# Kernel tuning notes

Measured on AMD Instinct MI355X. Metric: run time of the kernel, lower is better.

The kernel has to match this reference:

```python
import jax, jax.numpy as jnp
import numpy as np

N, NJ, K, F = 30000, 12, 32, 128


def _resmlp(x, wr, br, w1, b1):
    # Residual: x + Linear(SiLU(x)); then ResMLP head: Linear(SiLU(.))
    h = x + jax.nn.silu(x) @ wr.T + br
    return jax.nn.silu(h) @ w1.T + b1


def setup_inputs() -> dict:
    key = jax.random.key(0)
    ks = jax.random.split(key, 40)
    d = {}
    d["atom_fea"] = jax.random.normal(ks[0], (N, F), jnp.float32)
    d["nbr_fea_idx"] = jax.random.randint(ks[1], (N, NJ), 0, N)
    d["gs"] = jax.random.normal(ks[2], (N, NJ, K), jnp.float32)
    d["gp"] = jax.random.normal(ks[3], (N, NJ, K, 3), jnp.float32)
    d["gd"] = jax.random.normal(ks[4], (N, NJ, K, 5), jnp.float32)
    # parameters (nn.init.uniform_ default is U[0,1); scaled down for stability)
    d["Gs"] = jax.random.uniform(ks[5], (F, K), jnp.float32) * 0.1
    d["Gp"] = jax.random.uniform(ks[6], (F, K), jnp.float32) * 0.1
    d["Gd"] = jax.random.uniform(ks[7], (F, K), jnp.float32) * 0.1
    d["P1"] = jax.random.uniform(ks[8], (F, F), jnp.float32) * 0.02
    d["P2"] = jax.random.uniform(ks[9], (F, F), jnp.float32) * 0.02
    d["D1"] = jax.random.uniform(ks[10], (F, F), jnp.float32) * 0.02
    d["D2"] = jax.random.uniform(ks[11], (F, F), jnp.float32) * 0.02
    i = 12
    for name in ("c", "s", "p", "d"):
        d[name + "_wr"] = jax.random.normal(ks[i], (F, F), jnp.float32) * 0.05; i += 1
        d[name + "_br"] = jnp.zeros((F,), jnp.float32)
        d[name + "_w1"] = jax.random.normal(ks[i], (F, F), jnp.float32) * 0.05; i += 1
        d[name + "_b1"] = jnp.zeros((F,), jnp.float32)
    return d


def reference(atom_fea, nbr_fea_idx, gs, gp, gd,
              Gs, Gp, Gd, P1, P2, D1, D2,
              c_wr, c_br, c_w1, c_b1,
              s_wr, s_br, s_w1, s_b1,
              p_wr, p_br, p_w1, p_b1,
              d_wr, d_br, d_w1, d_b1):
    s_fea = _resmlp(atom_fea, s_wr, s_br, s_w1, s_b1)  # (N,F)
    p_fea = _resmlp(atom_fea, p_wr, p_br, p_w1, p_b1)
    d_fea = _resmlp(atom_fea, d_wr, d_br, d_w1, d_b1)

    # s channel: env_j = Gs @ gs_j, si = sum_j s_fea[nbr_j] * env_j
    env_s = jnp.einsum('fk,njk->njf', Gs, gs)                 # (N,NJ,F)
    final_s = jnp.sum(s_fea[nbr_fea_idx] * env_s, axis=1)     # (N,F)

    # p channel: (N,F,3) per-atom, then trace((P2^T p^T)(p P1)) = sum(pP1 * pP2)
    env_p = jnp.einsum('fk,njka->njfa', Gp, gp)               # (N,NJ,F,3)
    all_p = jnp.sum(p_fea[nbr_fea_idx][..., None] * env_p, axis=1)  # (N,F,3)
    all_p = jnp.swapaxes(all_p, 1, 2)                          # (N,3,F)
    p1 = jnp.einsum('naf,fg->nag', all_p, P1)
    p2 = jnp.einsum('naf,fg->nag', all_p, P2)
    final_p = jnp.sum(p1 * p2, axis=(1, 2))[:, None]           # (N,1) -> bcast (N,F)

    # d channel: same with 5 components
    env_d = jnp.einsum('fk,njka->njfa', Gd, gd)               # (N,NJ,F,5)
    all_d = jnp.sum(d_fea[nbr_fea_idx][..., None] * env_d, axis=1)  # (N,F,5)
    all_d = jnp.swapaxes(all_d, 1, 2)                          # (N,5,F)
    d1 = jnp.einsum('naf,fg->nag', all_d, D1)
    d2 = jnp.einsum('naf,fg->nag', all_d, D2)
    final_d = jnp.sum(d1 * d2, axis=(1, 2))[:, None]

    final_c = _resmlp(atom_fea, c_wr, c_br, c_w1, c_b1)        # (N,F)
    return final_c + final_s + final_p + final_d
```

## Files before the change

### kernel.cpp

```cpp
#include <hip/hip_runtime.h>

#define N_ATOMS 30000
#define NJ 12
#define FDIM 128

typedef __attribute__((ext_vector_type(8))) short short8;
typedef __attribute__((ext_vector_type(4))) float f32x4;

#define WFRAG_OFF 0
#define GFRAG_OFF 262144
#define MFRAG_OFF 286720
#define FEA_OFF   483328
#define FEA_ELEMS 3840000
#define ALLP_OFF  23523328
#define ALLD_OFF  46563328
#define QP_OFF    84963328
#define QD_OFF    85323328

__device__ __forceinline__ unsigned pack_bf2(float a, float b){
  unsigned r;
  asm("v_cvt_pk_bf16_f32 %0, %1, %2" : "=v"(r) : "v"(a), "v"(b));
  return r;
}
__device__ __forceinline__ unsigned short f2b(float f){
  return (unsigned short)pack_bf2(f, 0.f);
}
__device__ __forceinline__ float b2f(unsigned short s){
  unsigned u = ((unsigned)s) << 16;
  return __builtin_bit_cast(float, u);
}
__device__ __forceinline__ float silu_f(float x){ return x / (1.0f + __expf(-x)); }
__device__ __forceinline__ void lds_fence(){
  __builtin_amdgcn_sched_barrier(0);
  asm volatile("s_waitcnt lgkmcnt(0)" ::: "memory");
  __builtin_amdgcn_sched_barrier(0);
}
__device__ __forceinline__ short8 frag4(unsigned d0, unsigned d1, unsigned d2, unsigned d3, bool valid){
  if (!valid){ d0 = 0u; d1 = 0u; d2 = 0u; d3 = 0u; }
  uint4 u; u.x = d0; u.y = d1; u.z = d2; u.w = d3;
  return __builtin_bit_cast(short8, u);
}

struct Ptr8 { const float* p[8]; };
struct Ptr3 { const float* p[3]; };
struct Bias { const float* br[4]; const float* b1[4]; };

__global__ __launch_bounds__(256) void k_prep(
    const float* __restrict__ P1, const float* __restrict__ P2,
    const float* __restrict__ D1, const float* __restrict__ D2,
    Ptr8 w8, Ptr3 g3, char* __restrict__ ws)
{
  int b = blockIdx.x, t = threadIdx.x;
  if (b < 16){
    int mat = b >> 3, rb = b & 7;
    const float* A = mat ? D1 : P1;
    const float* B = mat ? D2 : P2;
    unsigned short* dst = (unsigned short*)(ws + MFRAG_OFF) + (size_t)mat*16384;
    for (int it = 0; it < 8; ++it){
      int o = it*256 + t;
      int row = rb*16 + (o >> 7), col = o & 127;
      const float4* ar = (const float4*)(A + (size_t)row*128);
      const float4* br = (const float4*)(B + (size_t)col*128);
      float s = 0.f;
      #pragma unroll 8
      for (int q = 0; q < 32; ++q){
        float4 a = ar[q], c = br[q];
        s += a.x*c.x + a.y*c.y + a.z*c.z + a.w*c.w;
      }
      int ks = row >> 5, ft = col >> 4;
      int ln = (col & 15) | (((row >> 3) & 3) << 4);
      dst[(size_t)(((ks*8 + ft)*64 + ln)*8 + (row & 7))] = f2b(s);
    }
  } else if (b < 24){
    int mat = b - 16;
    const float* W = w8.p[mat];
    unsigned short* dst = (unsigned short*)(ws + WFRAG_OFF) + (size_t)mat*16384;
    for (int it = 0; it < 64; ++it){
      int idx = it*256 + t;
      int i = idx & 7, ln = (idx >> 3) & 63, ft = (idx >> 9) & 7, ks = idx >> 12;
      int f = ft*16 + (ln & 15);
      int k = ks*32 + ((ln >> 4) & 3)*8 + i;
      dst[idx] = f2b(W[(size_t)f*128 + k]);
    }
  } else {
    int mat = b - 24;
    const float* G = g3.p[mat];
    unsigned short* dst = (unsigned short*)(ws + GFRAG_OFF) + (size_t)mat*4096;
    for (int it = 0; it < 16; ++it){
      int idx = it*256 + t;
      int i = idx & 7, ln = (idx >> 3) & 63, ft = idx >> 9;
      int f = ft*16 + (ln & 15);
      int k = ((ln >> 4) & 3)*8 + i;
      dst[idx] = f2b(G[(size_t)f*32 + k]);
    }
  }
}

__global__ __launch_bounds__(256) void k_resmlp(
    const float* __restrict__ x, char* __restrict__ ws, Bias bs,
    float* __restrict__ out)
{
  __shared__ alignas(16) char sm[32768];
  const int tid = threadIdx.x, lane = tid & 63;
  const int wid = __builtin_amdgcn_readfirstlane(tid >> 6);
  const int lo = lane & 15, hi = lane >> 4;
  const int ch = blockIdx.y;
  const int rowbase = (int)blockIdx.x*64 + wid*16;
  char* xL = sm + wid*8192;
  char* hL = xL + 4096;

  #pragma unroll
  for (int it = 0; it < 8; ++it){
    int e4 = it*64 + lane;
    int row = e4 >> 5, k0 = (e4 & 31)*4;
    int grow = rowbase + row; if (grow >= N_ATOMS) grow = N_ATOMS-1;
    float4 v = *(const float4*)(x + (size_t)grow*FDIM + k0);
    uint2 u;
    u.x = pack_bf2(silu_f(v.x), silu_f(v.y));
    u.y = pack_bf2(silu_f(v.z), silu_f(v.w));
    int ks = k0 >> 5, h2 = (k0 >> 3) & 3, i0 = k0 & 7, lanep = row | (h2 << 4);
    *(uint2*)(xL + ks*1024 + lanep*16 + i0*2) = u;
  }
  lds_fence();
  short8 A[4];
  #pragma unroll
  for (int ks = 0; ks < 4; ++ks) A[ks] = *(const short8*)(xL + ks*1024 + lane*16);

  const char* wrp = ws + (size_t)(ch*2)*32768;
  const char* w1p = ws + (size_t)(ch*2 + 1)*32768;
  const float* brp = bs.br[ch];
  const float* b1p = bs.b1[ch];

  f32x4 acc[8];
  #pragma unroll
  for (int ft = 0; ft < 8; ++ft) acc[ft] = (f32x4){0.f,0.f,0.f,0.f};
  #pragma unroll
  for (int ks = 0; ks < 4; ++ks){
    #pragma unroll
    for (int ft = 0; ft < 8; ++ft){
      short8 B = *(const short8*)(wrp + (size_t)(((ks*8 + ft)*64 + lane)*16));
      acc[ft] = __builtin_amdgcn_mfma_f32_16x16x32_bf16(A[ks], B, acc[ft], 0, 0, 0);
    }
  }
  #pragma unroll
  for (int ft = 0; ft < 8; ++ft){
    int f = ft*16 + lo;
    float bias = brp[f];
    #pragma unroll
    for (int r = 0; r < 4; ++r){
      int grow = rowbase + hi*4 + r; if (grow >= N_ATOMS) grow = N_ATOMS-1;
      float h = acc[ft][r] + x[(size_t)grow*FDIM + f] + bias;
      float sh = silu_f(h);
      int ks2 = f >> 5, h2 = (f >> 3) & 3, i2 = f & 7, lanep = (hi*4 + r) | (h2 << 4);
      *(unsigned short*)(hL + ks2*1024 + lanep*16 + i2*2) = f2b(sh);
    }
  }
  lds_fence();
  short8 A2[4];
  #pragma unroll
  for (int ks = 0; ks < 4; ++ks) A2[ks] = *(const short8*)(hL + ks*1024 + lane*16);

  f32x4 acc2[8];
  #pragma unroll
  for (int ft = 0; ft < 8; ++ft) acc2[ft] = (f32x4){0.f,0.f,0.f,0.f};
  #pragma unroll
  for (int ks = 0; ks < 4; ++ks){
    #pragma unroll
    for (int ft = 0; ft < 8; ++ft){
      short8 B = *(const short8*)(w1p + (size_t)(((ks*8 + ft)*64 + lane)*16));
      acc2[ft] = __builtin_amdgcn_mfma_f32_16x16x32_bf16(A2[ks], B, acc2[ft], 0, 0, 0);
    }
  }
  if (ch == 0){
    #pragma unroll
    for (int ft = 0; ft < 8; ++ft){
      int f = ft*16 + lo;
      float bb = b1p[f];
      #pragma unroll
      for (int r = 0; r < 4; ++r){
        int grow = rowbase + hi*4 + r; if (grow >= N_ATOMS) grow = N_ATOMS-1;
        out[(size_t)grow*FDIM + f] = acc2[ft][r] + bb;
      }
    }
  } else {
    unsigned short* fea = (unsigned short*)(ws + FEA_OFF) + (size_t)(ch-1)*FEA_ELEMS;
    #pragma unroll
    for (int ft = 0; ft < 8; ++ft){
      int f = ft*16 + lo;
      float bb = b1p[f];
      #pragma unroll
      for (int r = 0; r < 4; ++r){
        int grow = rowbase + hi*4 + r; if (grow >= N_ATOMS) grow = N_ATOMS-1;
        fea[(size_t)grow*FDIM + f] = f2b(acc2[ft][r] + bb);
      }
    }
  }
}

#define FPAD 264
#define SLABROWS 40
#define SLAB (SLABROWS*FPAD)

__device__ __forceinline__ void stage_fea(char* buf, const unsigned short* fea,
                                          int nb, int lane)
{
  #pragma unroll
  for (int j = 0; j < NJ; ++j){
    int nj = __builtin_amdgcn_readlane(nb, j);
    const unsigned* rp = (const unsigned*)(fea + (size_t)nj*FDIM);
    unsigned v = rp[lane];
    *(unsigned*)(buf + j*FPAD + lane*4) = v;
  }
}

__global__ __launch_bounds__(256, 4) void k_chan(
    const float* __restrict__ gs, const float* __restrict__ gp,
    const float* __restrict__ gd, const int* __restrict__ nbr,
    char* __restrict__ ws, float* __restrict__ out)
{
  __shared__ alignas(16) char sm[4*SLAB];
  const int tid = threadIdx.x, lane = tid & 63;
  const int wid = __builtin_amdgcn_readfirstlane(tid >> 6);
  const int lo = lane & 15, hi = lane >> 4;
  const bool jvalid = lo < NJ;
  const int jc = jvalid ? lo : NJ-1;
  char* slab = sm + wid*SLAB;
  const int atom = (int)blockIdx.x*4 + wid;
  const f32x4 z4 = {0.f,0.f,0.f,0.f};
  const unsigned short* feaS = (const unsigned short*)(ws + FEA_OFF);
  const char* gfrag = ws + GFRAG_OFF;

  int nb = 0;
  if (lane < NJ) nb = nbr[(size_t)atom*NJ + lane];

  #pragma unroll
  for (int t = 0; t < 4; ++t)
    *(float*)(slab + 36*FPAD + (t*64 + lane)*4) = 0.f;
  if (lane < 8) *(float*)(slab + 36*FPAD + 1024 + lane*4) = 0.f;

  stage_fea(slab,            feaS,               nb, lane);
  stage_fea(slab + 12*FPAD,  feaS + FEA_ELEMS,   nb, lane);
  stage_fea(slab + 24*FPAD,  feaS + 2*FEA_ELEMS, nb, lane);

  const float* gsp = gs + (size_t)atom*384 + (jc*32 + hi*8);
  f32x4 sv0 = *(const f32x4*)(gsp);
  f32x4 sv1 = *(const f32x4*)(gsp + 4);
  const float* gpp = gp + (size_t)atom*1152 + (jc*96 + hi*24);
  float pr[24];
  #pragma unroll
  for (int q = 0; q < 6; ++q){
    f32x4 v = *(const f32x4*)(gpp + q*4);
    #pragma unroll
    for (int c2 = 0; c2 < 4; ++c2) pr[q*4+c2] = v[c2];
  }

  const char* a0s = slab + hi*(4*FPAD) + lo*2;

  lds_fence();

  {
    short8 AfS = frag4(pack_bf2(sv0[0],sv0[1]), pack_bf2(sv0[2],sv0[3]),
                       pack_bf2(sv1[0],sv1[1]), pack_bf2(sv1[2],sv1[3]), jvalid);
    short8 Bg[8];
    #pragma unroll
    for (int ft = 0; ft < 8; ++ft)
      Bg[ft] = *(const short8*)(gfrag + (size_t)((ft*64 + lane)*16));
    float outv0 = 0.f, outv1 = 0.f;
    #pragma unroll
    for (int ft = 0; ft < 8; ++ft){
      float w0 = b2f(*(const unsigned short*)(a0s + 0*FPAD + ft*32));
      float w1 = b2f(*(const unsigned short*)(a0s + 1*FPAD + ft*32));
      float w2 = b2f(*(const unsigned short*)(a0s + 2*FPAD + ft*32));
      float w3 = b2f(*(const unsigned short*)(a0s + 3*FPAD + ft*32));
      f32x4 c = __builtin_amdgcn_mfma_f32_16x16x32_bf16(AfS, Bg[ft], z4, 0, 0, 0);
      float p = c[0]*w0 + c[1]*w1 + c[2]*w2 + c[3]*w3;
      p += __shfl_xor(p, 16);
      p += __shfl_xor(p, 32);
      if (ft == hi)     outv0 += p;
      if (ft == hi + 4) outv1 += p;
    }
    size_t ob = (size_t)atom*FDIM;
    out[ob + lane]      += outv0;
    out[ob + 64 + lane] += outv1;
  }

  const float* gdp = gd + (size_t)atom*1920 + (jc*160 + hi*40);
  float dr[40];
  #pragma unroll
  for (int q = 0; q < 10; ++q){
    f32x4 v = *(const f32x4*)(gdp + q*4);
    #pragma unroll
    for (int c2 = 0; c2 < 4; ++c2) dr[q*4+c2] = v[c2];
  }

  {
    unsigned short* allp = (unsigned short*)(ws + ALLP_OFF);
    short8 AfP[3];
    #pragma unroll
    for (int a = 0; a < 3; ++a)
      AfP[a] = frag4(pack_bf2(pr[0+a],pr[3+a]),   pack_bf2(pr[6+a],pr[9+a]),
                     pack_bf2(pr[12+a],pr[15+a]), pack_bf2(pr[18+a],pr[21+a]), jvalid);
    short8 Bg[8];
    #pragma unroll
    for (int ft = 0; ft < 8; ++ft)
      Bg[ft] = *(const short8*)(gfrag + 8192 + (size_t)((ft*64 + lane)*16));
    const char* a0 = a0s + 12*FPAD;
    #pragma unroll
    for (int ft = 0; ft < 8; ++ft){
      float w0 = b2f(*(const unsigned short*)(a0 + 0*FPAD + ft*32));
      float w1 = b2f(*(const unsigned short*)(a0 + 1*FPAD + ft*32));
      float w2 = b2f(*(const unsigned short*)(a0 + 2*FPAD + ft*32));
      float w3 = b2f(*(const unsigned short*)(a0 + 3*FPAD + ft*32));
      #pragma unroll
      for (int a = 0; a < 3; ++a){
        f32x4 c = __builtin_amdgcn_mfma_f32_16x16x32_bf16(AfP[a], Bg[ft], z4, 0, 0, 0);
        float p = c[0]*w0 + c[1]*w1 + c[2]*w2 + c[3]*w3;
        p += __shfl_xor(p, 16);
        p += __shfl_xor(p, 32);
        if (lane < 16)
          allp[(size_t)(atom*3 + a)*FDIM + ft*16 + lane] = f2b(p);
      }
    }
  }

  {
    unsigned short* alld = (unsigned short*)(ws + ALLD_OFF);
    short8 AfD[5];
    #pragma unroll
    for (int a = 0; a < 5; ++a)
      AfD[a] = frag4(pack_bf2(dr[0+a],dr[5+a]),   pack_bf2(dr[10+a],dr[15+a]),
                     pack_bf2(dr[20+a],dr[25+a]), pack_bf2(dr[30+a],dr[35+a]), jvalid);
    short8 Bg[8];
    #pragma unroll
    for (int ft = 0; ft < 8; ++ft)
      Bg[ft] = *(const short8*)(gfrag + 16384 + (size_t)((ft*64 + lane)*16));
    const char* a0 = a0s + 24*FPAD;
    #pragma unroll
    for (int ft = 0; ft < 8; ++ft){
      float w0 = b2f(*(const unsigned short*)(a0 + 0*FPAD + ft*32));
      float w1 = b2f(*(const unsigned short*)(a0 + 1*FPAD + ft*32));
      float w2 = b2f(*(const unsigned short*)(a0 + 2*FPAD + ft*32));
      float w3 = b2f(*(const unsigned short*)(a0 + 3*FPAD + ft*32));
      #pragma unroll
      for (int a = 0; a < 5; ++a){
        f32x4 c = __builtin_amdgcn_mfma_f32_16x16x32_bf16(AfD[a], Bg[ft], z4, 0, 0, 0);
        float p = c[0]*w0 + c[1]*w1 + c[2]*w2 + c[3]*w3;
        p += __shfl_xor(p, 16);
        p += __shfl_xor(p, 32);
        if (lane < 16)
          alld[(size_t)(atom*5 + a)*FDIM + ft*16 + lane] = f2b(p);
      }
    }
  }
}

__global__ __launch_bounds__(256) void k_quad(char* __restrict__ ws)
{
  __shared__ alignas(16) char mB[32768];
  const int tid = threadIdx.x, lane = tid & 63;
  const int wid = __builtin_amdgcn_readfirstlane(tid >> 6);
  const int lo = lane & 15, hi = lane >> 4;
  const int mat = blockIdx.y;
  const f32x4* msrc = (const f32x4*)(ws + MFRAG_OFF + (size_t)mat*32768);
  #pragma unroll
  for (int it = 0; it < 8; ++it)
    *((f32x4*)mB + it*256 + tid) = msrc[it*256 + tid];
  __syncthreads();

  const char* rows = ws + (mat ? ALLD_OFF : ALLP_OFF);
  float* qdst = (float*)(ws + (mat ? QD_OFF : QP_OFF));
  const int ntiles = mat ? (N_ATOMS*5)/16 : (N_ATOMS*3)/16;
  const int nw = (int)gridDim.x*4;

  for (int t = (int)blockIdx.x*4 + wid; t < ntiles; t += nw){
    const int rowb = t*16;
    short8 Aq[4];
    #pragma unroll
    for (int ks = 0; ks < 4; ++ks)
      Aq[ks] = *(const short8*)(rows + (size_t)(rowb + lo)*256 + ks*64 + hi*16);
    unsigned short vv[8][4];
    #pragma unroll
    for (int ft = 0; ft < 8; ++ft)
      #pragma unroll
      for (int r = 0; r < 4; ++r)
        vv[ft][r] = *(const unsigned short*)(rows + (size_t)(rowb + hi*4 + r)*256 + (ft*16 + lo)*2);

    f32x4 acc[8];
    #pragma unroll
    for (int ft = 0; ft < 8; ++ft) acc[ft] = (f32x4){0.f,0.f,0.f,0.f};
    #pragma unroll
    for (int ks = 0; ks < 4; ++ks){
      #pragma unroll
      for (int ft = 0; ft < 8; ++ft){
        short8 B = *(const short8*)(mB + (size_t)(((ks*8 + ft)*64 + lane)*16));
        acc[ft] = __builtin_amdgcn_mfma_f32_16x16x32_bf16(Aq[ks], B, acc[ft], 0, 0, 0);
      }
    }
    float part[4] = {0.f,0.f,0.f,0.f};
    #pragma unroll
    for (int ft = 0; ft < 8; ++ft)
      #pragma unroll
      for (int r = 0; r < 4; ++r)
        part[r] += acc[ft][r] * b2f(vv[ft][r]);
    #pragma unroll
    for (int r = 0; r < 4; ++r){
      #pragma unroll
      for (int m = 1; m < 16; m <<= 1) part[r] += __shfl_xor(part[r], m);
    }
    if (lo == 0){
      #pragma unroll
      for (int r = 0; r < 4; ++r) qdst[rowb + hi*4 + r] = part[r];
    }
  }
}

__global__ __launch_bounds__(256) void k_final(char* __restrict__ ws,
                                               float* __restrict__ out)
{
  const float* qp = (const float*)(ws + QP_OFF);
  const float* qd = (const float*)(ws + QD_OFF);
  int e = (int)blockIdx.x*256 + threadIdx.x;
  int i = e >> 7;
  float q = qp[i*3] + qp[i*3+1] + qp[i*3+2]
          + qd[i*5] + qd[i*5+1] + qd[i*5+2] + qd[i*5+3] + qd[i*5+4];
  out[e] += q;
}

extern "C" void kernel_launch(void* const* d_in, const int* in_sizes, int n_in,
                              void* d_out, int out_size, void* d_ws, size_t ws_size,
                              hipStream_t stream)
{
  const float* atom_fea = (const float*)d_in[0];
  const int*   nbr      = (const int*)d_in[1];
  const float* gs = (const float*)d_in[2];
  const float* gp = (const float*)d_in[3];
  const float* gd = (const float*)d_in[4];
  const float* Gs = (const float*)d_in[5];
  const float* Gp = (const float*)d_in[6];
  const float* Gd = (const float*)d_in[7];
  const float* P1 = (const float*)d_in[8];
  const float* P2 = (const float*)d_in[9];
  const float* D1 = (const float*)d_in[10];
  const float* D2 = (const float*)d_in[11];

  Ptr8 w8;
  w8.p[0] = (const float*)d_in[12];
  w8.p[1] = (const float*)d_in[14];
  w8.p[2] = (const float*)d_in[16];
  w8.p[3] = (const float*)d_in[18];
  w8.p[4] = (const float*)d_in[20];
  w8.p[5] = (const float*)d_in[22];
  w8.p[6] = (const float*)d_in[24];
  w8.p[7] = (const float*)d_in[26];
  Ptr3 g3; g3.p[0] = Gs; g3.p[1] = Gp; g3.p[2] = Gd;
  Bias bs;
  bs.br[0] = (const float*)d_in[13]; bs.b1[0] = (const float*)d_in[15];
  bs.br[1] = (const float*)d_in[17]; bs.b1[1] = (const float*)d_in[19];
  bs.br[2] = (const float*)d_in[21]; bs.b1[2] = (const float*)d_in[23];
  bs.br[3] = (const float*)d_in[25]; bs.b1[3] = (const float*)d_in[27];

  char* ws = (char*)d_ws;
  float* out = (float*)d_out;

  k_prep  <<<27, 256, 0, stream>>>(P1, P2, D1, D2, w8, g3, ws);
  dim3 g1((N_ATOMS + 63)/64, 4);
  k_resmlp<<<g1, 256, 0, stream>>>(atom_fea, ws, bs, out);
  k_chan  <<<N_ATOMS/4, 256, 0, stream>>>(gs, gp, gd, nbr, ws, out);
  dim3 gq(256, 2);
  k_quad  <<<gq, 256, 0, stream>>>(ws);
  k_final <<<15000, 256, 0, stream>>>(ws, out);
}
```

Baseline: 282.1 us.

## Reuse one LDS slab per channel and prefetch neighbor features into registers

Shrinks the per-wave LDS slab from three channel regions (40 rows) to a single 16-row region that is reused for the s, p and d channels in turn. Neighbor feature gathers for the next channel are issued into registers early, so their global latency overlaps the MFMA work of the current channel, and they are written to LDS just before use. Scheduling barriers keep the stores in place. The smaller LDS footprint may allow more resident blocks, at the cost of extra VGPRs for the prefetch buffers.

Result: faster. 266.6 us (-5.5%).

```diff
diff --git a/kernel.cpp b/kernel.cpp
--- a/kernel.cpp
+++ b/kernel.cpp
@@ -198,20 +198,7 @@
 }
 
 #define FPAD 264
-#define SLABROWS 40
-#define SLAB (SLABROWS*FPAD)
-
-__device__ __forceinline__ void stage_fea(char* buf, const unsigned short* fea,
-                                          int nb, int lane)
-{
-  #pragma unroll
-  for (int j = 0; j < NJ; ++j){
-    int nj = __builtin_amdgcn_readlane(nb, j);
-    const unsigned* rp = (const unsigned*)(fea + (size_t)nj*FDIM);
-    unsigned v = rp[lane];
-    *(unsigned*)(buf + j*FPAD + lane*4) = v;
-  }
-}
+#define SLAB (16*FPAD)
 
 __global__ __launch_bounds__(256, 4) void k_chan(
     const float* __restrict__ gs, const float* __restrict__ gp,
@@ -228,6 +215,8 @@
   const int atom = (int)blockIdx.x*4 + wid;
   const f32x4 z4 = {0.f,0.f,0.f,0.f};
   const unsigned short* feaS = (const unsigned short*)(ws + FEA_OFF);
+  const unsigned short* feaP = feaS + FEA_ELEMS;
+  const unsigned short* feaD = feaS + 2*FEA_ELEMS;
   const char* gfrag = ws + GFRAG_OFF;
 
   int nb = 0;
@@ -235,12 +224,20 @@
 
   #pragma unroll
   for (int t = 0; t < 4; ++t)
-    *(float*)(slab + 36*FPAD + (t*64 + lane)*4) = 0.f;
-  if (lane < 8) *(float*)(slab + 36*FPAD + 1024 + lane*4) = 0.f;
-
-  stage_fea(slab,            feaS,               nb, lane);
-  stage_fea(slab + 12*FPAD,  feaS + FEA_ELEMS,   nb, lane);
-  stage_fea(slab + 24*FPAD,  feaS + 2*FEA_ELEMS, nb, lane);
+    *(float*)(slab + 12*FPAD + (t*64 + lane)*4) = 0.f;
+  if (lane < 8) *(float*)(slab + 12*FPAD + 1024 + lane*4) = 0.f;
+
+  unsigned gS[NJ], gP[NJ];
+  #pragma unroll
+  for (int j = 0; j < NJ; ++j){
+    int nj = __builtin_amdgcn_readlane(nb, j);
+    gS[j] = ((const unsigned*)(feaS + (size_t)nj*FDIM))[lane];
+  }
+  #pragma unroll
+  for (int j = 0; j < NJ; ++j){
+    int nj = __builtin_amdgcn_readlane(nb, j);
+    gP[j] = ((const unsigned*)(feaP + (size_t)nj*FDIM))[lane];
+  }
 
   const float* gsp = gs + (size_t)atom*384 + (jc*32 + hi*8);
   f32x4 sv0 = *(const f32x4*)(gsp);
@@ -256,8 +253,10 @@
 
   const char* a0s = slab + hi*(4*FPAD) + lo*2;
 
+  #pragma unroll
+  for (int j = 0; j < NJ; ++j)
+    *(unsigned*)(slab + j*FPAD + lane*4) = gS[j];
   lds_fence();
-
   {
     short8 AfS = frag4(pack_bf2(sv0[0],sv0[1]), pack_bf2(sv0[2],sv0[3]),
                        pack_bf2(sv1[0],sv1[1]), pack_bf2(sv1[2],sv1[3]), jvalid);
@@ -284,6 +283,19 @@
     out[ob + 64 + lane] += outv1;
   }
 
+  unsigned gD[NJ];
+  #pragma unroll
+  for (int j = 0; j < NJ; ++j){
+    int nj = __builtin_amdgcn_readlane(nb, j);
+    gD[j] = ((const unsigned*)(feaD + (size_t)nj*FDIM))[lane];
+  }
+
+  __builtin_amdgcn_sched_barrier(0);
+  #pragma unroll
+  for (int j = 0; j < NJ; ++j)
+    *(unsigned*)(slab + j*FPAD + lane*4) = gP[j];
+  lds_fence();
+
   const float* gdp = gd + (size_t)atom*1920 + (jc*160 + hi*40);
   float dr[40];
   #pragma unroll
@@ -304,13 +316,12 @@
     #pragma unroll
     for (int ft = 0; ft < 8; ++ft)
       Bg[ft] = *(const short8*)(gfrag + 8192 + (size_t)((ft*64 + lane)*16));
-    const char* a0 = a0s + 12*FPAD;
-    #pragma unroll
-    for (int ft = 0; ft < 8; ++ft){
-      float w0 = b2f(*(const unsigned short*)(a0 + 0*FPAD + ft*32));
-      float w1 = b2f(*(const unsigned short*)(a0 + 1*FPAD + ft*32));
-      float w2 = b2f(*(const unsigned short*)(a0 + 2*FPAD + ft*32));
-      float w3 = b2f(*(const unsigned short*)(a0 + 3*FPAD + ft*32));
+    #pragma unroll
+    for (int ft = 0; ft < 8; ++ft){
+      float w0 = b2f(*(const unsigned short*)(a0s + 0*FPAD + ft*32));
+      float w1 = b2f(*(const unsigned short*)(a0s + 1*FPAD + ft*32));
+      float w2 = b2f(*(const unsigned short*)(a0s + 2*FPAD + ft*32));
+      float w3 = b2f(*(const unsigned short*)(a0s + 3*FPAD + ft*32));
       #pragma unroll
       for (int a = 0; a < 3; ++a){
         f32x4 c = __builtin_amdgcn_mfma_f32_16x16x32_bf16(AfP[a], Bg[ft], z4, 0, 0, 0);
@@ -323,6 +334,11 @@
     }
   }
 
+  __builtin_amdgcn_sched_barrier(0);
+  #pragma unroll
+  for (int j = 0; j < NJ; ++j)
+    *(unsigned*)(slab + j*FPAD + lane*4) = gD[j];
+  lds_fence();
   {
     unsigned short* alld = (unsigned short*)(ws + ALLD_OFF);
     short8 AfD[5];
@@ -334,13 +350,12 @@
     #pragma unroll
     for (int ft = 0; ft < 8; ++ft)
       Bg[ft] = *(const short8*)(gfrag + 16384 + (size_t)((ft*64 + lane)*16));
-    const char* a0 = a0s + 24*FPAD;
-    #pragma unroll
-    for (int ft = 0; ft < 8; ++ft){
-      float w0 = b2f(*(const unsigned short*)(a0 + 0*FPAD + ft*32));
-      float w1 = b2f(*(const unsigned short*)(a0 + 1*FPAD + ft*32));
-      float w2 = b2f(*(const unsigned short*)(a0 + 2*FPAD + ft*32));
-      float w3 = b2f(*(const unsigned short*)(a0 + 3*FPAD + ft*32));
+    #pragma unroll
+    for (int ft = 0; ft < 8; ++ft){
+      float w0 = b2f(*(const unsigned short*)(a0s + 0*FPAD + ft*32));
+      float w1 = b2f(*(const unsigned short*)(a0s + 1*FPAD + ft*32));
+      float w2 = b2f(*(const unsigned short*)(a0s + 2*FPAD + ft*32));
+      float w3 = b2f(*(const unsigned short*)(a0s + 3*FPAD + ft*32));
       #pragma unroll
       for (int a = 0; a < 5; ++a){
         f32x4 c = __builtin_amdgcn_mfma_f32_16x16x32_bf16(AfD[a], Bg[ft], z4, 0, 0, 0);
```

## Split channel kernel per channel, process 4 atoms per wave with prefetched gathers

Applied to the files above, without the earlier changes.

The channel kernel is split across a grid y-dimension so each block handles one of the s/p/d channels. Each wave now loops over 4 atoms and gathers the next atom's neighbor rows into registers while the current atom's MFMAs run, which shrinks the LDS slab and hoists the G fragment loads out of the per-atom work. A separate small kernel pre-reduces the per-atom p/d quadratic terms so the final kernel only reads one float per atom. Costs: one extra launch, the neighbor index list is read three times, and more registers are needed for the prefetch buffers.

After: 267.2 us. -5.3%, faster.

```diff
diff --git a/kernel.cpp b/kernel.cpp
--- a/kernel.cpp
+++ b/kernel.cpp
@@ -16,6 +16,7 @@
 #define ALLD_OFF  46563328
 #define QP_OFF    84963328
 #define QD_OFF    85323328
+#define QSUM_OFF  85923328
 
 __device__ __forceinline__ unsigned pack_bf2(float a, float b){
   unsigned r;
@@ -198,18 +199,111 @@
 }
 
 #define FPAD 264
-#define SLABROWS 40
-#define SLAB (SLABROWS*FPAD)
-
-__device__ __forceinline__ void stage_fea(char* buf, const unsigned short* fea,
-                                          int nb, int lane)
+#define SLAB 4224
+
+__device__ __forceinline__ void gather_rows(unsigned (&gN)[NJ],
+    const unsigned short* fea, int nb, int lane)
 {
   #pragma unroll
   for (int j = 0; j < NJ; ++j){
     int nj = __builtin_amdgcn_readlane(nb, j);
-    const unsigned* rp = (const unsigned*)(fea + (size_t)nj*FDIM);
-    unsigned v = rp[lane];
-    *(unsigned*)(buf + j*FPAD + lane*4) = v;
+    gN[j] = ((const unsigned*)(fea + (size_t)nj*FDIM))[lane];
+  }
+}
+
+template<int CH>
+__device__ __forceinline__ void chan_run(
+    const float* __restrict__ g, const int* __restrict__ nbr,
+    char* __restrict__ ws, float* __restrict__ out,
+    char* slab, int a0, int lane, int lo, int hi, int jc, bool jvalid)
+{
+  constexpr int NA   = (CH == 0) ? 1 : ((CH == 1) ? 3 : 5);
+  constexpr int GSTR = (CH == 0) ? 384 : ((CH == 1) ? 1152 : 1920);
+  constexpr int PERJ = GSTR / NJ;
+  const unsigned short* fea = (const unsigned short*)(ws + FEA_OFF) + (size_t)CH*FEA_ELEMS;
+  const char* gfrag = ws + GFRAG_OFF + CH*8192;
+  unsigned short* rows_out = (unsigned short*)(ws + ((CH == 1) ? ALLP_OFF : ALLD_OFF));
+  const f32x4 z4 = {0.f,0.f,0.f,0.f};
+
+  #pragma unroll
+  for (int t = 0; t < 4; ++t)
+    *(float*)(slab + NJ*FPAD + (t*64 + lane)*4) = 0.f;
+  if (lane < 8) *(float*)(slab + NJ*FPAD + 1024 + lane*4) = 0.f;
+
+  short8 Bg[8];
+  #pragma unroll
+  for (int ft = 0; ft < 8; ++ft)
+    Bg[ft] = *(const short8*)(gfrag + (size_t)((ft*64 + lane)*16));
+
+  int nbn = 0;
+  {
+    int nb = 0;
+    if (lane < NJ) nb = nbr[(size_t)a0*NJ + lane];
+    unsigned g0[NJ];
+    gather_rows(g0, fea, nb, lane);
+    #pragma unroll
+    for (int j = 0; j < NJ; ++j)
+      *(unsigned*)(slab + j*FPAD + lane*4) = g0[j];
+    int a1 = a0 + 1; if (a1 > N_ATOMS-1) a1 = N_ATOMS-1;
+    if (lane < NJ) nbn = nbr[(size_t)a1*NJ + lane];
+  }
+  const char* a0p = slab + hi*(4*FPAD) + lo*2;
+
+  #pragma unroll 1
+  for (int i = 0; i < 4; ++i){
+    const int a = a0 + i;
+    const float* gp_ = g + (size_t)a*GSTR + (jc*PERJ + hi*(PERJ/4));
+    float raw[NA*8];
+    #pragma unroll
+    for (int q = 0; q < NA*2; ++q){
+      f32x4 v = *(const f32x4*)(gp_ + q*4);
+      raw[q*4+0] = v[0]; raw[q*4+1] = v[1]; raw[q*4+2] = v[2]; raw[q*4+3] = v[3];
+    }
+    unsigned gNn[NJ];
+    gather_rows(gNn, fea, nbn, lane);
+    int nb2 = 0;
+    { int a2 = a + 2; if (a2 > N_ATOMS-1) a2 = N_ATOMS-1;
+      if (lane < NJ) nb2 = nbr[(size_t)a2*NJ + lane]; }
+    lds_fence();
+    short8 Af[NA];
+    #pragma unroll
+    for (int aa = 0; aa < NA; ++aa)
+      Af[aa] = frag4(pack_bf2(raw[0*NA+aa], raw[1*NA+aa]),
+                     pack_bf2(raw[2*NA+aa], raw[3*NA+aa]),
+                     pack_bf2(raw[4*NA+aa], raw[5*NA+aa]),
+                     pack_bf2(raw[6*NA+aa], raw[7*NA+aa]), jvalid);
+    float outv0 = 0.f, outv1 = 0.f;
+    #pragma unroll
+    for (int ft = 0; ft < 8; ++ft){
+      float w0 = b2f(*(const unsigned short*)(a0p + 0*FPAD + ft*32));
+      float w1 = b2f(*(const unsigned short*)(a0p + 1*FPAD + ft*32));
+      float w2 = b2f(*(const unsigned short*)(a0p + 2*FPAD + ft*32));
+      float w3 = b2f(*(const unsigned short*)(a0p + 3*FPAD + ft*32));
+      #pragma unroll
+      for (int aa = 0; aa < NA; ++aa){
+        f32x4 c = __builtin_amdgcn_mfma_f32_16x16x32_bf16(Af[aa], Bg[ft], z4, 0, 0, 0);
+        float p = c[0]*w0 + c[1]*w1 + c[2]*w2 + c[3]*w3;
+        p += __shfl_xor(p, 16);
+        p += __shfl_xor(p, 32);
+        if (CH == 0){
+          if (ft == hi)     outv0 += p;
+          if (ft == hi + 4) outv1 += p;
+        } else {
+          if (lane < 16)
+            rows_out[(size_t)(a*NA + aa)*FDIM + ft*16 + lane] = f2b(p);
+        }
+      }
+    }
+    if (CH == 0){
+      size_t ob = (size_t)a*FDIM;
+      out[ob + lane]      += outv0;
+      out[ob + 64 + lane] += outv1;
+    }
+    __builtin_amdgcn_sched_barrier(0);
+    #pragma unroll
+    for (int j = 0; j < NJ; ++j)
+      *(unsigned*)(slab + j*FPAD + lane*4) = gNn[j];
+    nbn = nb2;
   }
 }
 
@@ -225,133 +319,12 @@
   const bool jvalid = lo < NJ;
   const int jc = jvalid ? lo : NJ-1;
   char* slab = sm + wid*SLAB;
-  const int atom = (int)blockIdx.x*4 + wid;
-  const f32x4 z4 = {0.f,0.f,0.f,0.f};
-  const unsigned short* feaS = (const unsigned short*)(ws + FEA_OFF);
-  const char* gfrag = ws + GFRAG_OFF;
-
-  int nb = 0;
-  if (lane < NJ) nb = nbr[(size_t)atom*NJ + lane];
-
-  #pragma unroll
-  for (int t = 0; t < 4; ++t)
-    *(float*)(slab + 36*FPAD + (t*64 + lane)*4) = 0.f;
-  if (lane < 8) *(float*)(slab + 36*FPAD + 1024 + lane*4) = 0.f;
-
-  stage_fea(slab,            feaS,               nb, lane);
-  stage_fea(slab + 12*FPAD,  feaS + FEA_ELEMS,   nb, lane);
-  stage_fea(slab + 24*FPAD,  feaS + 2*FEA_ELEMS, nb, lane);
-
-  const float* gsp = gs + (size_t)atom*384 + (jc*32 + hi*8);
-  f32x4 sv0 = *(const f32x4*)(gsp);
-  f32x4 sv1 = *(const f32x4*)(gsp + 4);
-  const float* gpp = gp + (size_t)atom*1152 + (jc*96 + hi*24);
-  float pr[24];
-  #pragma unroll
-  for (int q = 0; q < 6; ++q){
-    f32x4 v = *(const f32x4*)(gpp + q*4);
-    #pragma unroll
-    for (int c2 = 0; c2 < 4; ++c2) pr[q*4+c2] = v[c2];
-  }
-
-  const char* a0s = slab + hi*(4*FPAD) + lo*2;
-
-  lds_fence();
-
-  {
-    short8 AfS = frag4(pack_bf2(sv0[0],sv0[1]), pack_bf2(sv0[2],sv0[3]),
-                       pack_bf2(sv1[0],sv1[1]), pack_bf2(sv1[2],sv1[3]), jvalid);
-    short8 Bg[8];
-    #pragma unroll
-    for (int ft = 0; ft < 8; ++ft)
-      Bg[ft] = *(const short8*)(gfrag + (size_t)((ft*64 + lane)*16));
-    float outv0 = 0.f, outv1 = 0.f;
-    #pragma unroll
-    for (int ft = 0; ft < 8; ++ft){
-      float w0 = b2f(*(const unsigned short*)(a0s + 0*FPAD + ft*32));
-      float w1 = b2f(*(const unsigned short*)(a0s + 1*FPAD + ft*32));
-      float w2 = b2f(*(const unsigned short*)(a0s + 2*FPAD + ft*32));
-      float w3 = b2f(*(const unsigned short*)(a0s + 3*FPAD + ft*32));
-      f32x4 c = __builtin_amdgcn_mfma_f32_16x16x32_bf16(AfS, Bg[ft], z4, 0, 0, 0);
-      float p = c[0]*w0 + c[1]*w1 + c[2]*w2 + c[3]*w3;
-      p += __shfl_xor(p, 16);
-      p += __shfl_xor(p, 32);
-      if (ft == hi)     outv0 += p;
-      if (ft == hi + 4) outv1 += p;
-    }
-    size_t ob = (size_t)atom*FDIM;
-    out[ob + lane]      += outv0;
-    out[ob + 64 + lane] += outv1;
-  }
-
-  const float* gdp = gd + (size_t)atom*1920 + (jc*160 + hi*40);
-  float dr[40];
-  #pragma unroll
-  for (int q = 0; q < 10; ++q){
-    f32x4 v = *(const f32x4*)(gdp + q*4);
-    #pragma unroll
-    for (int c2 = 0; c2 < 4; ++c2) dr[q*4+c2] = v[c2];
-  }
-
-  {
-    unsigned short* allp = (unsigned short*)(ws + ALLP_OFF);
-    short8 AfP[3];
-    #pragma unroll
-    for (int a = 0; a < 3; ++a)
-      AfP[a] = frag4(pack_bf2(pr[0+a],pr[3+a]),   pack_bf2(pr[6+a],pr[9+a]),
-                     pack_bf2(pr[12+a],pr[15+a]), pack_bf2(pr[18+a],pr[21+a]), jvalid);
-    short8 Bg[8];
-    #pragma unroll
-    for (int ft = 0; ft < 8; ++ft)
-      Bg[ft] = *(const short8*)(gfrag + 8192 + (size_t)((ft*64 + lane)*16));
-    const char* a0 = a0s + 12*FPAD;
-    #pragma unroll
-    for (int ft = 0; ft < 8; ++ft){
-      float w0 = b2f(*(const unsigned short*)(a0 + 0*FPAD + ft*32));
-      float w1 = b2f(*(const unsigned short*)(a0 + 1*FPAD + ft*32));
-      float w2 = b2f(*(const unsigned short*)(a0 + 2*FPAD + ft*32));
-      float w3 = b2f(*(const unsigned short*)(a0 + 3*FPAD + ft*32));
-      #pragma unroll
-      for (int a = 0; a < 3; ++a){
-        f32x4 c = __builtin_amdgcn_mfma_f32_16x16x32_bf16(AfP[a], Bg[ft], z4, 0, 0, 0);
-        float p = c[0]*w0 + c[1]*w1 + c[2]*w2 + c[3]*w3;
-        p += __shfl_xor(p, 16);
-        p += __shfl_xor(p, 32);
-        if (lane < 16)
-          allp[(size_t)(atom*3 + a)*FDIM + ft*16 + lane] = f2b(p);
-      }
-    }
-  }
-
-  {
-    unsigned short* alld = (unsigned short*)(ws + ALLD_OFF);
-    short8 AfD[5];
-    #pragma unroll
-    for (int a = 0; a < 5; ++a)
-      AfD[a] = frag4(pack_bf2(dr[0+a],dr[5+a]),   pack_bf2(dr[10+a],dr[15+a]),
-                     pack_bf2(dr[20+a],dr[25+a]), pack_bf2(dr[30+a],dr[35+a]), jvalid);
-    short8 Bg[8];
-    #pragma unroll
-    for (int ft = 0; ft < 8; ++ft)
-      Bg[ft] = *(const short8*)(gfrag + 16384 + (size_t)((ft*64 + lane)*16));
-    const char* a0 = a0s + 24*FPAD;
-    #pragma unroll
-    for (int ft = 0; ft < 8; ++ft){
-      float w0 = b2f(*(const unsigned short*)(a0 + 0*FPAD + ft*32));
-      float w1 = b2f(*(const unsigned short*)(a0 + 1*FPAD + ft*32));
-      float w2 = b2f(*(const unsigned short*)(a0 + 2*FPAD + ft*32));
-      float w3 = b2f(*(const unsigned short*)(a0 + 3*FPAD + ft*32));
-      #pragma unroll
-      for (int a = 0; a < 5; ++a){
-        f32x4 c = __builtin_amdgcn_mfma_f32_16x16x32_bf16(AfD[a], Bg[ft], z4, 0, 0, 0);
-        float p = c[0]*w0 + c[1]*w1 + c[2]*w2 + c[3]*w3;
-        p += __shfl_xor(p, 16);
-        p += __shfl_xor(p, 32);
-        if (lane < 16)
-          alld[(size_t)(atom*5 + a)*FDIM + ft*16 + lane] = f2b(p);
-      }
-    }
-  }
+  const int a0 = ((int)blockIdx.x*4 + wid)*4;
+  const int ch = (int)blockIdx.y;
+
+  if (ch == 0)      chan_run<0>(gs, nbr, ws, out, slab, a0, lane, lo, hi, jc, jvalid);
+  else if (ch == 1) chan_run<1>(gp, nbr, ws, out, slab, a0, lane, lo, hi, jc, jvalid);
+  else              chan_run<2>(gd, nbr, ws, out, slab, a0, lane, lo, hi, jc, jvalid);
 }
 
 __global__ __launch_bounds__(256) void k_quad(char* __restrict__ ws)
@@ -414,16 +387,23 @@
   }
 }
 
+__global__ __launch_bounds__(256) void k_qred(char* __restrict__ ws)
+{
+  int i = (int)blockIdx.x*256 + threadIdx.x;
+  if (i >= N_ATOMS) return;
+  const float* qp = (const float*)(ws + QP_OFF);
+  const float* qd = (const float*)(ws + QD_OFF);
+  float q = qp[i*3] + qp[i*3+1] + qp[i*3+2]
+          + qd[i*5] + qd[i*5+1] + qd[i*5+2] + qd[i*5+3] + qd[i*5+4];
+  ((float*)(ws + QSUM_OFF))[i] = q;
+}
+
 __global__ __launch_bounds__(256) void k_final(char* __restrict__ ws,
                                                float* __restrict__ out)
 {
-  const float* qp = (const float*)(ws + QP_OFF);
-  const float* qd = (const float*)(ws + QD_OFF);
+  const float* qsum = (const float*)(ws + QSUM_OFF);
   int e = (int)blockIdx.x*256 + threadIdx.x;
-  int i = e >> 7;
-  float q = qp[i*3] + qp[i*3+1] + qp[i*3+2]
-          + qd[i*5] + qd[i*5+1] + qd[i*5+2] + qd[i*5+3] + qd[i*5+4];
-  out[e] += q;
+  out[e] += qsum[e >> 7];
 }
 
 extern "C" void kernel_launch(void* const* d_in, const int* in_sizes, int n_in,
@@ -465,8 +445,10 @@
   k_prep  <<<27, 256, 0, stream>>>(P1, P2, D1, D2, w8, g3, ws);
   dim3 g1((N_ATOMS + 63)/64, 4);
   k_resmlp<<<g1, 256, 0, stream>>>(atom_fea, ws, bs, out);
-  k_chan  <<<N_ATOMS/4, 256, 0, stream>>>(gs, gp, gd, nbr, ws, out);
+  dim3 gc(N_ATOMS/16, 3);
+  k_chan  <<<gc, 256, 0, stream>>>(gs, gp, gd, nbr, ws, out);
   dim3 gq(256, 2);
   k_quad  <<<gq, 256, 0, stream>>>(ws);
+  k_qred  <<<(N_ATOMS + 255)/256, 256, 0, stream>>>(ws);
   k_final <<<15000, 256, 0, stream>>>(ws, out);
 }
```
